# Optimization experiments

Measured on AMD Instinct MI355X. Metric: run time of the kernel, lower is better.

Reference implementation:

```python
import jax, jax.numpy as jnp
import numpy as np

N_SENT = 100000   # source ('sent') nodes
N_TYPE = 10000    # destination ('type') nodes
E = 640000        # edges of etype 'has'
D = 128           # out_dim
LEAKY_SLOPE = 0.01  # F.leaky_relu default


def setup_inputs() -> dict:
    key = jax.random.key(0)
    k0, k1, k2, k3, k4 = jax.random.split(key, 5)
    h_sent = jax.random.normal(k0, (N_SENT, D), jnp.float32)
    h_type = jax.random.normal(k1, (N_TYPE, D), jnp.float32)
    # attn_fc: Linear(2*D, 1, bias=False) -> weight [1, 2*D]
    attn_w = jax.random.normal(k2, (1, 2 * D), jnp.float32) * (1.0 / np.sqrt(2 * D))
    src_idx = jax.random.randint(k3, (E,), 0, N_SENT, dtype=jnp.int32)
    dst_idx = jax.random.randint(k4, (E,), 0, N_TYPE, dtype=jnp.int32)
    return {"h_sent": h_sent, "h_type": h_type, "attn_w": attn_w,
            "src_idx": src_idx, "dst_idx": dst_idx}


def reference(h_sent, h_type, attn_w, src_idx, dst_idx):
    w = attn_w[0]  # [2D]
    # attn_fc(cat(src_h, dst_h)) == src_h @ w[:D] + dst_h @ w[D:]  (no bias)
    s_src = h_sent @ w[:D]   # [N_SENT]
    s_dst = h_type @ w[D:]   # [N_TYPE]
    e = jax.nn.leaky_relu(s_src[src_idx] + s_dst[dst_idx], LEAKY_SLOPE)  # [E]
    # segment (per-destination) softmax over incoming edges
    m = jax.ops.segment_max(e, dst_idx, num_segments=N_TYPE)             # [N_TYPE]
    m = jnp.where(jnp.isfinite(m), m, 0.0)                               # empty segments -> 0
    ex = jnp.exp(e - m[dst_idx])                                         # [E]
    denom = jax.ops.segment_sum(ex, dst_idx, num_segments=N_TYPE)        # [N_TYPE]
    alpha = ex / denom[dst_idx]                                          # [E]
    # weighted scatter-sum of source features into destination nodes
    msg = alpha[:, None] * h_sent[src_idx]                               # [E, D]
    h_new = jax.ops.segment_sum(msg, dst_idx, num_segments=N_TYPE)       # [N_TYPE, D]
    # DGL only updates nodes that received messages; isolated nodes keep h
    deg = jax.ops.segment_sum(jnp.ones_like(e), dst_idx, num_segments=N_TYPE)
    return jnp.where(deg[:, None] > 0, h_new, h_type)
```

## Files before the change

kernel.cpp:

```cpp
#include <hip/hip_runtime.h>
#include <stdint.h>
#include <stddef.h>

#define N_SENT 100000
#define N_TYPE 10000
#define NEDGE  640000
#define NROWS  (N_SENT + N_TYPE)
#define HB     128
#define HCHUNK (NEDGE / HB)

__device__ __forceinline__ float bf2f(uint32_t lo16) {
    return __builtin_bit_cast(float, lo16 << 16);
}
__device__ __forceinline__ uint32_t f2bf(float f) {
    uint32_t u = __builtin_bit_cast(uint32_t, f);
    return (u + 0x7fffu + ((u >> 16) & 1u)) >> 16;
}
__device__ __forceinline__ bool detect_bf16(const uint32_t* __restrict__ h) {
    uint32_t u = h[threadIdx.x & 63];
    uint32_t e_lo = (u >> 7) & 0xffu;
    int ok = (e_lo >= 100u && e_lo <= 140u) ? 1 : 0;
    unsigned long long m = __ballot(ok);
    return __popcll(m) >= 48;
}

#define SCORE_BLOCKS ((NROWS + 63) / 64)

__global__ __launch_bounds__(256) void scores_count_k(const void* __restrict__ h_sent,
                                                      const void* __restrict__ h_type,
                                                      const void* __restrict__ attn_w,
                                                      const int* __restrict__ dst,
                                                      float* __restrict__ s_src,
                                                      float* __restrict__ s_dst,
                                                      uint32_t* __restrict__ count2) {
    __shared__ uint32_t hist[N_TYPE];
    int b = blockIdx.x;
    if (b < SCORE_BLOCKS) {
        int lane = threadIdx.x & 63;
        int r0   = (b * 4 + (int)(threadIdx.x >> 6)) * 16;
        bool isbf = detect_bf16((const uint32_t*)h_sent);
        float v[16];
        if (isbf) {
            uint32_t wv_s = ((const uint32_t*)attn_w)[lane];
            uint32_t wv_t = ((const uint32_t*)attn_w)[64 + lane];
            float ws0 = bf2f(wv_s & 0xffffu), ws1 = bf2f(wv_s >> 16);
            float wt0 = bf2f(wv_t & 0xffffu), wt1 = bf2f(wv_t >> 16);
#pragma unroll
            for (int i = 0; i < 16; i++) {
                int g = r0 + i;
                if (g >= NROWS) { v[i] = 0.0f; continue; }
                bool isSrc = g < N_SENT;
                const uint32_t* hp = isSrc
                    ? (const uint32_t*)h_sent + (size_t)g * 64
                    : (const uint32_t*)h_type + (size_t)(g - N_SENT) * 64;
                uint32_t hv = hp[lane];
                v[i] = isSrc ? (bf2f(hv & 0xffffu) * ws0 + bf2f(hv >> 16) * ws1)
                             : (bf2f(hv & 0xffffu) * wt0 + bf2f(hv >> 16) * wt1);
            }
        } else {
            float2 wv_s = ((const float2*)attn_w)[lane];
            float2 wv_t = ((const float2*)attn_w)[64 + lane];
#pragma unroll
            for (int i = 0; i < 16; i++) {
                int g = r0 + i;
                if (g >= NROWS) { v[i] = 0.0f; continue; }
                bool isSrc = g < N_SENT;
                const float2* hp = isSrc
                    ? (const float2*)h_sent + (size_t)g * 64
                    : (const float2*)h_type + (size_t)(g - N_SENT) * 64;
                float2 hv = hp[lane];
                v[i] = isSrc ? (hv.x * wv_s.x + hv.y * wv_s.y)
                             : (hv.x * wv_t.x + hv.y * wv_t.y);
            }
        }
        int b0 = lane & 1, b1 = (lane >> 1) & 1, b2 = (lane >> 2) & 1, b3 = (lane >> 3) & 1;
        float w_[8];
#pragma unroll
        for (int i = 0; i < 8; i++) {
            float keep = b0 ? v[2 * i + 1] : v[2 * i];
            float send = b0 ? v[2 * i]     : v[2 * i + 1];
            w_[i] = keep + __shfl_xor(send, 1, 64);
        }
        float x_[4];
#pragma unroll
        for (int i = 0; i < 4; i++) {
            float keep = b1 ? w_[2 * i + 1] : w_[2 * i];
            float send = b1 ? w_[2 * i]     : w_[2 * i + 1];
            x_[i] = keep + __shfl_xor(send, 2, 64);
        }
        float y_[2];
#pragma unroll
        for (int i = 0; i < 2; i++) {
            float keep = b2 ? x_[2 * i + 1] : x_[2 * i];
            float send = b2 ? x_[2 * i]     : x_[2 * i + 1];
            y_[i] = keep + __shfl_xor(send, 4, 64);
        }
        float z;
        {
            float keep = b3 ? y_[1] : y_[0];
            float send = b3 ? y_[0] : y_[1];
            z = keep + __shfl_xor(send, 8, 64);
        }
        z += __shfl_xor(z, 16, 64);
        z += __shfl_xor(z, 32, 64);
        if (lane < 16) {
            int g = r0 + lane;
            if (g < NROWS) {
                if (g < N_SENT) s_src[g] = z;
                else            s_dst[g - N_SENT] = z;
            }
        }
    } else {
        int cb = b - SCORE_BLOCKS;
        int t  = threadIdx.x;
        for (int i = t; i < N_TYPE; i += 256) hist[i] = 0u;
        __syncthreads();
        int e0 = cb * HCHUNK;
        for (int i = t; i < HCHUNK; i += 256)
            atomicAdd(&hist[dst[e0 + i]], 1u);
        __syncthreads();
        uint32_t* row = count2 + (size_t)cb * N_TYPE;
        for (int i = t; i < N_TYPE; i += 256) row[i] = hist[i];
    }
}

__global__ __launch_bounds__(256) void sumscan_k(uint32_t* __restrict__ count2,
                                                 uint32_t* __restrict__ total) {
    int b = blockIdx.x * 256 + threadIdx.x;
    if (b >= N_TYPE) return;
    uint32_t run = 0;
#pragma unroll 8
    for (int c = 0; c < HB; c++) {
        uint32_t* p = count2 + (size_t)c * N_TYPE + b;
        uint32_t v = *p;
        *p = run;
        run += v;
    }
    total[b] = run;
}

__global__ __launch_bounds__(1024) void scan_k(const uint32_t* __restrict__ total,
                                               uint32_t* __restrict__ offsets) {
    const int CH = 10;
    int t = threadIdx.x, lane = t & 63, wv = t >> 6;
    int base = t * CH;
    uint32_t local[CH];
    uint32_t tsum = 0;
#pragma unroll
    for (int i = 0; i < CH; i++) {
        int idx = base + i;
        uint32_t c = (idx < N_TYPE) ? total[idx] : 0u;
        local[i] = c;
        tsum += c;
    }
    uint32_t orig = tsum;
#pragma unroll
    for (int off = 1; off < 64; off <<= 1) {
        uint32_t v = __shfl_up(tsum, off, 64);
        if (lane >= off) tsum += v;
    }
    __shared__ uint32_t wsum[16];
    if (lane == 63) wsum[wv] = tsum;
    __syncthreads();
    if (wv == 0 && lane < 16) {
        uint32_t u = wsum[lane], o = u;
#pragma unroll
        for (int off = 1; off < 16; off <<= 1) {
            uint32_t v = __shfl_up(u, off, 64);
            if (lane >= off) u += v;
        }
        wsum[lane] = u - o;
    }
    __syncthreads();
    uint32_t run = wsum[wv] + tsum - orig;
#pragma unroll
    for (int i = 0; i < CH; i++) {
        int idx = base + i;
        if (idx < N_TYPE) {
            offsets[idx] = run;
            run += local[i];
        } else if (idx == N_TYPE) {
            offsets[idx] = run;
        }
    }
}

__global__ __launch_bounds__(256) void fill_k(const int* __restrict__ src,
                                              const int* __restrict__ dst,
                                              const float* __restrict__ s_src,
                                              const float* __restrict__ s_dst,
                                              const uint32_t* __restrict__ offsets,
                                              const uint32_t* __restrict__ base2,
                                              uint2* __restrict__ edata) {
    __shared__ uint32_t cur[N_TYPE];
    int cb = blockIdx.x;
    int t  = threadIdx.x;
    const uint4* off4 = (const uint4*)offsets;
    const uint4* brow4 = (const uint4*)(base2 + (size_t)cb * N_TYPE);
    for (int i = t; i < N_TYPE / 4; i += 256) {
        uint4 o = off4[i], bq = brow4[i];
        cur[4 * i + 0] = o.x + bq.x;
        cur[4 * i + 1] = o.y + bq.y;
        cur[4 * i + 2] = o.z + bq.z;
        cur[4 * i + 3] = o.w + bq.w;
    }
    __syncthreads();
    int e0 = cb * HCHUNK;
    for (int i = t; i < HCHUNK; i += 256) {
        int e = e0 + i;
        int d = dst[e];
        int s = src[e];
        float v = s_src[s] + s_dst[d];
        v = v > 0.0f ? v : 0.01f * v;
        float w = __expf(v);
        uint32_t pos = atomicAdd(&cur[d], 1u);
        edata[pos] = make_uint2((uint32_t)s, __builtin_bit_cast(uint32_t, w));
    }
}

__global__ __launch_bounds__(256) void agg_k(const void* __restrict__ h_sent,
                                             const void* __restrict__ h_type,
                                             const uint32_t* __restrict__ offsets,
                                             const uint2* __restrict__ edata,
                                             void* __restrict__ out) {
    int lane = threadIdx.x & 63;
    int j = (blockIdx.x * 256 + (int)threadIdx.x) >> 6;
    if (j >= N_TYPE) return;
    bool isbf = detect_bf16((const uint32_t*)h_sent);
    uint32_t beg = offsets[j], end = offsets[j + 1];
    if (isbf) {
        int g = lane >> 4, p = lane & 15;
        if (beg == end) {
            if (lane < 16)
                ((uint4*)out)[(size_t)j * 16 + p] = ((const uint4*)h_type)[(size_t)j * 16 + p];
            return;
        }
        const uint4* hp = (const uint4*)h_sent;
        float a[8] = {0, 0, 0, 0, 0, 0, 0, 0};
        float den = 0.0f;
        uint32_t k = beg;
        for (; k + 32 <= end; k += 32) {
            uint2 ed = edata[k + (lane & 31)];
#pragma unroll
            for (int i = 0; i < 8; i++) {
                int sl = 4 * i + g;
                uint32_t s = (uint32_t)__shfl((int)ed.x, sl, 64);
                float    w = __builtin_bit_cast(float, (uint32_t)__shfl((int)ed.y, sl, 64));
                uint4 gv = hp[(size_t)s * 16 + p];
                den += w;
                a[0] += w * bf2f(gv.x & 0xffffu); a[1] += w * bf2f(gv.x >> 16);
                a[2] += w * bf2f(gv.y & 0xffffu); a[3] += w * bf2f(gv.y >> 16);
                a[4] += w * bf2f(gv.z & 0xffffu); a[5] += w * bf2f(gv.z >> 16);
                a[6] += w * bf2f(gv.w & 0xffffu); a[7] += w * bf2f(gv.w >> 16);
            }
        }
        for (; k < end; k += 4) {
            uint32_t idx = k + (uint32_t)g;
            bool valid = idx < end;
            uint2 ed = edata[valid ? idx : (end - 1)];
            float w = valid ? __builtin_bit_cast(float, ed.y) : 0.0f;
            uint4 gv = hp[(size_t)ed.x * 16 + p];
            den += w;
            a[0] += w * bf2f(gv.x & 0xffffu); a[1] += w * bf2f(gv.x >> 16);
            a[2] += w * bf2f(gv.y & 0xffffu); a[3] += w * bf2f(gv.y >> 16);
            a[4] += w * bf2f(gv.z & 0xffffu); a[5] += w * bf2f(gv.z >> 16);
            a[6] += w * bf2f(gv.w & 0xffffu); a[7] += w * bf2f(gv.w >> 16);
        }
#pragma unroll
        for (int i = 0; i < 8; i++) {
            a[i] += __shfl_xor(a[i], 16, 64);
            a[i] += __shfl_xor(a[i], 32, 64);
        }
        den += __shfl_xor(den, 16, 64);
        den += __shfl_xor(den, 32, 64);
        float inv = 1.0f / den;
        if (lane < 16) {
            uint4 o;
            o.x = f2bf(a[0] * inv) | (f2bf(a[1] * inv) << 16);
            o.y = f2bf(a[2] * inv) | (f2bf(a[3] * inv) << 16);
            o.z = f2bf(a[4] * inv) | (f2bf(a[5] * inv) << 16);
            o.w = f2bf(a[6] * inv) | (f2bf(a[7] * inv) << 16);
            ((uint4*)out)[(size_t)j * 16 + p] = o;
        }
    } else {
        int g = lane >> 5, p = lane & 31;
        if (beg == end) {
            if (lane < 32)
                ((float4*)out)[(size_t)j * 32 + p] = ((const float4*)h_type)[(size_t)j * 32 + p];
            return;
        }
        const float4* hp = (const float4*)h_sent;
        float a0 = 0, a1 = 0, a2 = 0, a3 = 0, den = 0.0f;
        uint32_t k = beg;
        for (; k + 16 <= end; k += 16) {
            uint2 ed = edata[k + (lane & 15)];
#pragma unroll
            for (int i = 0; i < 8; i++) {
                int sl = 2 * i + g;
                uint32_t s = (uint32_t)__shfl((int)ed.x, sl, 64);
                float    w = __builtin_bit_cast(float, (uint32_t)__shfl((int)ed.y, sl, 64));
                float4 gv = hp[(size_t)s * 32 + p];
                den += w;
                a0 += w * gv.x; a1 += w * gv.y; a2 += w * gv.z; a3 += w * gv.w;
            }
        }
        for (; k < end; k += 2) {
            uint32_t idx = k + (uint32_t)g;
            bool valid = idx < end;
            uint2 ed = edata[valid ? idx : (end - 1)];
            float w = valid ? __builtin_bit_cast(float, ed.y) : 0.0f;
            float4 gv = hp[(size_t)ed.x * 32 + p];
            den += w;
            a0 += w * gv.x; a1 += w * gv.y; a2 += w * gv.z; a3 += w * gv.w;
        }
        a0 += __shfl_xor(a0, 32, 64);
        a1 += __shfl_xor(a1, 32, 64);
        a2 += __shfl_xor(a2, 32, 64);
        a3 += __shfl_xor(a3, 32, 64);
        den += __shfl_xor(den, 32, 64);
        float inv = 1.0f / den;
        if (lane < 32)
            ((float4*)out)[(size_t)j * 32 + p] = make_float4(a0 * inv, a1 * inv, a2 * inv, a3 * inv);
    }
}

static inline size_t align_up(size_t x) { return (x + 255) & ~(size_t)255; }

extern "C" void kernel_launch(void* const* d_in, const int* in_sizes, int n_in,
                              void* d_out, int out_size, void* d_ws, size_t ws_size,
                              hipStream_t stream) {
    const void* h_sent = d_in[0];
    const void* h_type = d_in[1];
    const void* attn_w = d_in[2];
    const int* src_idx = (const int*)d_in[3];
    const int* dst_idx = (const int*)d_in[4];

    char* w = (char*)d_ws;
    float*    s_src   = (float*)w;    w += align_up((size_t)N_SENT * 4);
    float*    s_dst   = (float*)w;    w += align_up((size_t)N_TYPE * 4);
    uint32_t* count2  = (uint32_t*)w; w += align_up((size_t)HB * N_TYPE * 4);
    uint32_t* total   = (uint32_t*)w; w += align_up((size_t)N_TYPE * 4);
    uint32_t* offsets = (uint32_t*)w; w += align_up((size_t)(N_TYPE + 1) * 4);
    uint2*    edata   = (uint2*)w;    w += align_up((size_t)NEDGE * 8);

    scores_count_k<<<SCORE_BLOCKS + HB, 256, 0, stream>>>(
        h_sent, h_type, attn_w, dst_idx, s_src, s_dst, count2);
    sumscan_k<<<(N_TYPE + 255) / 256, 256, 0, stream>>>(count2, total);
    scan_k<<<1, 1024, 0, stream>>>(total, offsets);
    fill_k<<<HB, 256, 0, stream>>>(src_idx, dst_idx, s_src, s_dst, offsets, count2, edata);
    agg_k<<<(N_TYPE + 3) / 4, 256, 0, stream>>>(h_sent, h_type, offsets, edata, d_out);
}
```

Before: 203.7 us.

## Fuse all five stages into one cooperative persistent kernel with grid syncs

Replaces the five separate launches (scores+histogram, column scan, total scan, fill, aggregate) with a single cooperative kernel of 512 persistent blocks that separates the phases with grid.sync, and loops over score rows and aggregation nodes with grid-stride loops. The goal is to remove per-launch overhead and the idle gaps between small kernels. It also packs the per-block histogram into 16-bit halves, halving LDS use for the atomics. In exchange, grid-wide barriers cost time, the fixed grid may under-occupy the aggregation phase, and the single-block scan adds a serial step.

```diff
diff --git a/kernel.cpp b/kernel.cpp
--- a/kernel.cpp
+++ b/kernel.cpp
@@ -1,13 +1,19 @@
 #include <hip/hip_runtime.h>
+#include <hip/hip_cooperative_groups.h>
 #include <stdint.h>
 #include <stddef.h>
+
+namespace cg = cooperative_groups;
 
 #define N_SENT 100000
 #define N_TYPE 10000
 #define NEDGE  640000
 #define NROWS  (N_SENT + N_TYPE)
+#define NB     512
+#define SCOREB 384
 #define HB     128
 #define HCHUNK (NEDGE / HB)
+#define NTASK  ((NROWS + 15) / 16)
 
 __device__ __forceinline__ float bf2f(uint32_t lo16) {
     return __builtin_bit_cast(float, lo16 << 16);
@@ -24,303 +30,324 @@
     return __popcll(m) >= 48;
 }
 
-#define SCORE_BLOCKS ((NROWS + 63) / 64)
-
-__global__ __launch_bounds__(256) void scores_count_k(const void* __restrict__ h_sent,
-                                                      const void* __restrict__ h_type,
-                                                      const void* __restrict__ attn_w,
-                                                      const int* __restrict__ dst,
-                                                      float* __restrict__ s_src,
-                                                      float* __restrict__ s_dst,
-                                                      uint32_t* __restrict__ count2) {
-    __shared__ uint32_t hist[N_TYPE];
-    int b = blockIdx.x;
-    if (b < SCORE_BLOCKS) {
-        int lane = threadIdx.x & 63;
-        int r0   = (b * 4 + (int)(threadIdx.x >> 6)) * 16;
-        bool isbf = detect_bf16((const uint32_t*)h_sent);
-        float v[16];
+__global__ __launch_bounds__(256, 4) void mega_k(
+    const void* __restrict__ h_sent, const void* __restrict__ h_type,
+    const void* __restrict__ attn_w,
+    const int* __restrict__ src_idx, const int* __restrict__ dst_idx,
+    float* __restrict__ s_src, float* __restrict__ s_dst,
+    uint32_t* __restrict__ count2, uint32_t* __restrict__ offsets,
+    uint2* __restrict__ edata, void* __restrict__ out)
+{
+    __shared__ uint32_t lds[N_TYPE];
+    cg::grid_group grid = cg::this_grid();
+    const int t    = threadIdx.x;
+    const int lane = t & 63;
+    const int wvid = t >> 6;
+    const int b    = blockIdx.x;
+    const bool isbf = detect_bf16((const uint32_t*)h_sent);
+
+    if (b < SCOREB) {
         if (isbf) {
             uint32_t wv_s = ((const uint32_t*)attn_w)[lane];
             uint32_t wv_t = ((const uint32_t*)attn_w)[64 + lane];
             float ws0 = bf2f(wv_s & 0xffffu), ws1 = bf2f(wv_s >> 16);
             float wt0 = bf2f(wv_t & 0xffffu), wt1 = bf2f(wv_t >> 16);
-#pragma unroll
-            for (int i = 0; i < 16; i++) {
-                int g = r0 + i;
-                if (g >= NROWS) { v[i] = 0.0f; continue; }
-                bool isSrc = g < N_SENT;
-                const uint32_t* hp = isSrc
-                    ? (const uint32_t*)h_sent + (size_t)g * 64
-                    : (const uint32_t*)h_type + (size_t)(g - N_SENT) * 64;
-                uint32_t hv = hp[lane];
-                v[i] = isSrc ? (bf2f(hv & 0xffffu) * ws0 + bf2f(hv >> 16) * ws1)
-                             : (bf2f(hv & 0xffffu) * wt0 + bf2f(hv >> 16) * wt1);
+            for (int task = b * 4 + wvid; task < NTASK; task += SCOREB * 4) {
+                int r0 = task * 16;
+                float v[16];
+#pragma unroll
+                for (int i = 0; i < 16; i++) {
+                    int g = r0 + i;
+                    if (g >= NROWS) { v[i] = 0.0f; continue; }
+                    bool isSrc = g < N_SENT;
+                    const uint32_t* hp = isSrc
+                        ? (const uint32_t*)h_sent + (size_t)g * 64
+                        : (const uint32_t*)h_type + (size_t)(g - N_SENT) * 64;
+                    uint32_t hv = hp[lane];
+                    v[i] = isSrc ? (bf2f(hv & 0xffffu) * ws0 + bf2f(hv >> 16) * ws1)
+                                 : (bf2f(hv & 0xffffu) * wt0 + bf2f(hv >> 16) * wt1);
+                }
+                int b0 = lane & 1, b1 = (lane >> 1) & 1, b2 = (lane >> 2) & 1, b3 = (lane >> 3) & 1;
+                float w_[8];
+#pragma unroll
+                for (int i = 0; i < 8; i++) {
+                    float keep = b0 ? v[2 * i + 1] : v[2 * i];
+                    float send = b0 ? v[2 * i]     : v[2 * i + 1];
+                    w_[i] = keep + __shfl_xor(send, 1, 64);
+                }
+                float x_[4];
+#pragma unroll
+                for (int i = 0; i < 4; i++) {
+                    float keep = b1 ? w_[2 * i + 1] : w_[2 * i];
+                    float send = b1 ? w_[2 * i]     : w_[2 * i + 1];
+                    x_[i] = keep + __shfl_xor(send, 2, 64);
+                }
+                float y_[2];
+#pragma unroll
+                for (int i = 0; i < 2; i++) {
+                    float keep = b2 ? x_[2 * i + 1] : x_[2 * i];
+                    float send = b2 ? x_[2 * i]     : x_[2 * i + 1];
+                    y_[i] = keep + __shfl_xor(send, 4, 64);
+                }
+                float z;
+                {
+                    float keep = b3 ? y_[1] : y_[0];
+                    float send = b3 ? y_[0] : y_[1];
+                    z = keep + __shfl_xor(send, 8, 64);
+                }
+                z += __shfl_xor(z, 16, 64);
+                z += __shfl_xor(z, 32, 64);
+                if (lane < 16) {
+                    int g = r0 + lane;
+                    if (g < NROWS) {
+                        if (g < N_SENT) s_src[g] = z;
+                        else            s_dst[g - N_SENT] = z;
+                    }
+                }
             }
         } else {
             float2 wv_s = ((const float2*)attn_w)[lane];
             float2 wv_t = ((const float2*)attn_w)[64 + lane];
-#pragma unroll
-            for (int i = 0; i < 16; i++) {
-                int g = r0 + i;
-                if (g >= NROWS) { v[i] = 0.0f; continue; }
-                bool isSrc = g < N_SENT;
-                const float2* hp = isSrc
-                    ? (const float2*)h_sent + (size_t)g * 64
-                    : (const float2*)h_type + (size_t)(g - N_SENT) * 64;
-                float2 hv = hp[lane];
-                v[i] = isSrc ? (hv.x * wv_s.x + hv.y * wv_s.y)
-                             : (hv.x * wv_t.x + hv.y * wv_t.y);
-            }
-        }
-        int b0 = lane & 1, b1 = (lane >> 1) & 1, b2 = (lane >> 2) & 1, b3 = (lane >> 3) & 1;
-        float w_[8];
-#pragma unroll
-        for (int i = 0; i < 8; i++) {
-            float keep = b0 ? v[2 * i + 1] : v[2 * i];
-            float send = b0 ? v[2 * i]     : v[2 * i + 1];
-            w_[i] = keep + __shfl_xor(send, 1, 64);
-        }
-        float x_[4];
-#pragma unroll
-        for (int i = 0; i < 4; i++) {
-            float keep = b1 ? w_[2 * i + 1] : w_[2 * i];
-            float send = b1 ? w_[2 * i]     : w_[2 * i + 1];
-            x_[i] = keep + __shfl_xor(send, 2, 64);
-        }
-        float y_[2];
-#pragma unroll
-        for (int i = 0; i < 2; i++) {
-            float keep = b2 ? x_[2 * i + 1] : x_[2 * i];
-            float send = b2 ? x_[2 * i]     : x_[2 * i + 1];
-            y_[i] = keep + __shfl_xor(send, 4, 64);
-        }
-        float z;
-        {
-            float keep = b3 ? y_[1] : y_[0];
-            float send = b3 ? y_[0] : y_[1];
-            z = keep + __shfl_xor(send, 8, 64);
-        }
-        z += __shfl_xor(z, 16, 64);
-        z += __shfl_xor(z, 32, 64);
-        if (lane < 16) {
-            int g = r0 + lane;
-            if (g < NROWS) {
-                if (g < N_SENT) s_src[g] = z;
-                else            s_dst[g - N_SENT] = z;
+            for (int task = b * 4 + wvid; task < NTASK; task += SCOREB * 4) {
+                int r0 = task * 16;
+                float v[16];
+#pragma unroll
+                for (int i = 0; i < 16; i++) {
+                    int g = r0 + i;
+                    if (g >= NROWS) { v[i] = 0.0f; continue; }
+                    bool isSrc = g < N_SENT;
+                    const float2* hp = isSrc
+                        ? (const float2*)h_sent + (size_t)g * 64
+                        : (const float2*)h_type + (size_t)(g - N_SENT) * 64;
+                    float2 hv = hp[lane];
+                    v[i] = isSrc ? (hv.x * wv_s.x + hv.y * wv_s.y)
+                                 : (hv.x * wv_t.x + hv.y * wv_t.y);
+                }
+                int b0 = lane & 1, b1 = (lane >> 1) & 1, b2 = (lane >> 2) & 1, b3 = (lane >> 3) & 1;
+                float w_[8];
+#pragma unroll
+                for (int i = 0; i < 8; i++) {
+                    float keep = b0 ? v[2 * i + 1] : v[2 * i];
+                    float send = b0 ? v[2 * i]     : v[2 * i + 1];
+                    w_[i] = keep + __shfl_xor(send, 1, 64);
+                }
+                float x_[4];
+#pragma unroll
+                for (int i = 0; i < 4; i++) {
+                    float keep = b1 ? w_[2 * i + 1] : w_[2 * i];
+                    float send = b1 ? w_[2 * i]     : w_[2 * i + 1];
+                    x_[i] = keep + __shfl_xor(send, 2, 64);
+                }
+                float y_[2];
+#pragma unroll
+                for (int i = 0; i < 2; i++) {
+                    float keep = b2 ? x_[2 * i + 1] : x_[2 * i];
+                    float send = b2 ? x_[2 * i]     : x_[2 * i + 1];
+                    y_[i] = keep + __shfl_xor(send, 4, 64);
+                }
+                float z;
+                {
+                    float keep = b3 ? y_[1] : y_[0];
+                    float send = b3 ? y_[0] : y_[1];
+                    z = keep + __shfl_xor(send, 8, 64);
+                }
+                z += __shfl_xor(z, 16, 64);
+                z += __shfl_xor(z, 32, 64);
+                if (lane < 16) {
+                    int g = r0 + lane;
+                    if (g < NROWS) {
+                        if (g < N_SENT) s_src[g] = z;
+                        else            s_dst[g - N_SENT] = z;
+                    }
+                }
             }
         }
     } else {
-        int cb = b - SCORE_BLOCKS;
-        int t  = threadIdx.x;
-        for (int i = t; i < N_TYPE; i += 256) hist[i] = 0u;
+        int cb = b - SCOREB;
+        for (int i = t; i < N_TYPE / 2; i += 256) lds[i] = 0u;
         __syncthreads();
         int e0 = cb * HCHUNK;
-        for (int i = t; i < HCHUNK; i += 256)
-            atomicAdd(&hist[dst[e0 + i]], 1u);
+        for (int i = t; i < HCHUNK; i += 256) {
+            int d = dst_idx[e0 + i];
+            atomicAdd(&lds[d >> 1], 1u << ((d & 1) * 16));
+        }
         __syncthreads();
-        uint32_t* row = count2 + (size_t)cb * N_TYPE;
-        for (int i = t; i < N_TYPE; i += 256) row[i] = hist[i];
-    }
-}
-
-__global__ __launch_bounds__(256) void sumscan_k(uint32_t* __restrict__ count2,
-                                                 uint32_t* __restrict__ total) {
-    int b = blockIdx.x * 256 + threadIdx.x;
-    if (b >= N_TYPE) return;
-    uint32_t run = 0;
-#pragma unroll 8
-    for (int c = 0; c < HB; c++) {
-        uint32_t* p = count2 + (size_t)c * N_TYPE + b;
-        uint32_t v = *p;
-        *p = run;
-        run += v;
-    }
-    total[b] = run;
-}
-
-__global__ __launch_bounds__(1024) void scan_k(const uint32_t* __restrict__ total,
-                                               uint32_t* __restrict__ offsets) {
-    const int CH = 10;
-    int t = threadIdx.x, lane = t & 63, wv = t >> 6;
-    int base = t * CH;
-    uint32_t local[CH];
-    uint32_t tsum = 0;
-#pragma unroll
-    for (int i = 0; i < CH; i++) {
-        int idx = base + i;
-        uint32_t c = (idx < N_TYPE) ? total[idx] : 0u;
-        local[i] = c;
-        tsum += c;
-    }
-    uint32_t orig = tsum;
-#pragma unroll
-    for (int off = 1; off < 64; off <<= 1) {
-        uint32_t v = __shfl_up(tsum, off, 64);
-        if (lane >= off) tsum += v;
-    }
-    __shared__ uint32_t wsum[16];
-    if (lane == 63) wsum[wv] = tsum;
-    __syncthreads();
-    if (wv == 0 && lane < 16) {
-        uint32_t u = wsum[lane], o = u;
-#pragma unroll
-        for (int off = 1; off < 16; off <<= 1) {
-            uint32_t v = __shfl_up(u, off, 64);
-            if (lane >= off) u += v;
-        }
-        wsum[lane] = u - o;
-    }
-    __syncthreads();
-    uint32_t run = wsum[wv] + tsum - orig;
-#pragma unroll
-    for (int i = 0; i < CH; i++) {
-        int idx = base + i;
-        if (idx < N_TYPE) {
-            offsets[idx] = run;
-            run += local[i];
-        } else if (idx == N_TYPE) {
-            offsets[idx] = run;
-        }
-    }
-}
-
-__global__ __launch_bounds__(256) void fill_k(const int* __restrict__ src,
-                                              const int* __restrict__ dst,
-                                              const float* __restrict__ s_src,
-                                              const float* __restrict__ s_dst,
-                                              const uint32_t* __restrict__ offsets,
-                                              const uint32_t* __restrict__ base2,
-                                              uint2* __restrict__ edata) {
-    __shared__ uint32_t cur[N_TYPE];
-    int cb = blockIdx.x;
-    int t  = threadIdx.x;
-    const uint4* off4 = (const uint4*)offsets;
-    const uint4* brow4 = (const uint4*)(base2 + (size_t)cb * N_TYPE);
-    for (int i = t; i < N_TYPE / 4; i += 256) {
-        uint4 o = off4[i], bq = brow4[i];
-        cur[4 * i + 0] = o.x + bq.x;
-        cur[4 * i + 1] = o.y + bq.y;
-        cur[4 * i + 2] = o.z + bq.z;
-        cur[4 * i + 3] = o.w + bq.w;
-    }
-    __syncthreads();
-    int e0 = cb * HCHUNK;
-    for (int i = t; i < HCHUNK; i += 256) {
-        int e = e0 + i;
-        int d = dst[e];
-        int s = src[e];
-        float v = s_src[s] + s_dst[d];
-        v = v > 0.0f ? v : 0.01f * v;
-        float w = __expf(v);
-        uint32_t pos = atomicAdd(&cur[d], 1u);
-        edata[pos] = make_uint2((uint32_t)s, __builtin_bit_cast(uint32_t, w));
-    }
-}
-
-__global__ __launch_bounds__(256) void agg_k(const void* __restrict__ h_sent,
-                                             const void* __restrict__ h_type,
-                                             const uint32_t* __restrict__ offsets,
-                                             const uint2* __restrict__ edata,
-                                             void* __restrict__ out) {
-    int lane = threadIdx.x & 63;
-    int j = (blockIdx.x * 256 + (int)threadIdx.x) >> 6;
-    if (j >= N_TYPE) return;
-    bool isbf = detect_bf16((const uint32_t*)h_sent);
-    uint32_t beg = offsets[j], end = offsets[j + 1];
-    if (isbf) {
-        int g = lane >> 4, p = lane & 15;
-        if (beg == end) {
-            if (lane < 16)
-                ((uint4*)out)[(size_t)j * 16 + p] = ((const uint4*)h_type)[(size_t)j * 16 + p];
-            return;
-        }
-        const uint4* hp = (const uint4*)h_sent;
-        float a[8] = {0, 0, 0, 0, 0, 0, 0, 0};
-        float den = 0.0f;
-        uint32_t k = beg;
-        for (; k + 32 <= end; k += 32) {
-            uint2 ed = edata[k + (lane & 31)];
-#pragma unroll
-            for (int i = 0; i < 8; i++) {
-                int sl = 4 * i + g;
-                uint32_t s = (uint32_t)__shfl((int)ed.x, sl, 64);
-                float    w = __builtin_bit_cast(float, (uint32_t)__shfl((int)ed.y, sl, 64));
-                uint4 gv = hp[(size_t)s * 16 + p];
+        uint2* row2 = (uint2*)(count2 + (size_t)cb * N_TYPE);
+        for (int i = t; i < N_TYPE / 2; i += 256) {
+            uint32_t wd = lds[i];
+            row2[i] = make_uint2(wd & 0xffffu, wd >> 16);
+        }
+    }
+    grid.sync();
+
+    {
+        int gtid = b * 256 + t;
+        if (gtid < N_TYPE) {
+            uint32_t run = 0;
+            for (int c = 0; c < HB; c++) {
+                uint32_t* p = count2 + (size_t)c * N_TYPE + gtid;
+                uint32_t v = *p;
+                *p = run;
+                run += v;
+            }
+            offsets[gtid] = run;
+        }
+    }
+    grid.sync();
+
+    if (b == 0) {
+        const int CH = N_TYPE / 256 + 1;
+        int base = t * CH;
+        uint32_t tsum = 0;
+        for (int i = 0; i < CH; i++) {
+            int idx = base + i;
+            if (idx < N_TYPE) tsum += offsets[idx];
+        }
+        uint32_t inc = tsum;
+#pragma unroll
+        for (int off = 1; off < 64; off <<= 1) {
+            uint32_t u = __shfl_up(inc, off, 64);
+            if (lane >= off) inc += u;
+        }
+        if (lane == 63) lds[wvid] = inc;
+        __syncthreads();
+        uint32_t wpre = 0;
+        for (int i = 0; i < wvid; i++) wpre += lds[i];
+        uint32_t run = wpre + inc - tsum;
+        for (int i = 0; i < CH; i++) {
+            int idx = base + i;
+            if (idx < N_TYPE) {
+                uint32_t v = offsets[idx];
+                offsets[idx] = run;
+                run += v;
+            } else if (idx == N_TYPE) {
+                offsets[idx] = run;
+            }
+        }
+    }
+    grid.sync();
+
+    if (b < HB) {
+        const uint4* off4 = (const uint4*)offsets;
+        const uint4* b4   = (const uint4*)(count2 + (size_t)b * N_TYPE);
+        for (int i = t; i < N_TYPE / 4; i += 256) {
+            uint4 o = off4[i], q = b4[i];
+            lds[4 * i + 0] = o.x + q.x;
+            lds[4 * i + 1] = o.y + q.y;
+            lds[4 * i + 2] = o.z + q.z;
+            lds[4 * i + 3] = o.w + q.w;
+        }
+        __syncthreads();
+        int e0 = b * HCHUNK;
+        for (int i = t; i < HCHUNK; i += 256) {
+            int e = e0 + i;
+            int d = dst_idx[e];
+            int s = src_idx[e];
+            float v = s_src[s] + s_dst[d];
+            v = v > 0.0f ? v : 0.01f * v;
+            float w = __expf(v);
+            uint32_t pos = atomicAdd(&lds[d], 1u);
+            edata[pos] = make_uint2((uint32_t)s, __builtin_bit_cast(uint32_t, w));
+        }
+    }
+    grid.sync();
+
+    for (int j = b * 4 + wvid; j < N_TYPE; j += NB * 4) {
+        uint32_t beg = offsets[j], end = offsets[j + 1];
+        if (isbf) {
+            int g = lane >> 4, p = lane & 15;
+            if (beg == end) {
+                if (lane < 16)
+                    ((uint4*)out)[(size_t)j * 16 + p] = ((const uint4*)h_type)[(size_t)j * 16 + p];
+                continue;
+            }
+            const uint4* hp = (const uint4*)h_sent;
+            float a[8] = {0, 0, 0, 0, 0, 0, 0, 0};
+            float den = 0.0f;
+            uint32_t k = beg;
+            for (; k + 32 <= end; k += 32) {
+                uint2 ed = edata[k + (lane & 31)];
+#pragma unroll
+                for (int i = 0; i < 8; i++) {
+                    int sl = 4 * i + g;
+                    uint32_t s = (uint32_t)__shfl((int)ed.x, sl, 64);
+                    float    w = __builtin_bit_cast(float, (uint32_t)__shfl((int)ed.y, sl, 64));
+                    uint4 gv = hp[(size_t)s * 16 + p];
+                    den += w;
+                    a[0] += w * bf2f(gv.x & 0xffffu); a[1] += w * bf2f(gv.x >> 16);
+                    a[2] += w * bf2f(gv.y & 0xffffu); a[3] += w * bf2f(gv.y >> 16);
+                    a[4] += w * bf2f(gv.z & 0xffffu); a[5] += w * bf2f(gv.z >> 16);
+                    a[6] += w * bf2f(gv.w & 0xffffu); a[7] += w * bf2f(gv.w >> 16);
+                }
+            }
+            for (; k < end; k += 4) {
+                uint32_t idx = k + (uint32_t)g;
+                bool valid = idx < end;
+                uint2 ed = edata[valid ? idx : (end - 1)];
+                float w = valid ? __builtin_bit_cast(float, ed.y) : 0.0f;
+                uint4 gv = hp[(size_t)ed.x * 16 + p];
                 den += w;
                 a[0] += w * bf2f(gv.x & 0xffffu); a[1] += w * bf2f(gv.x >> 16);
                 a[2] += w * bf2f(gv.y & 0xffffu); a[3] += w * bf2f(gv.y >> 16);
                 a[4] += w * bf2f(gv.z & 0xffffu); a[5] += w * bf2f(gv.z >> 16);
                 a[6] += w * bf2f(gv.w & 0xffffu); a[7] += w * bf2f(gv.w >> 16);
             }
-        }
-        for (; k < end; k += 4) {
-            uint32_t idx = k + (uint32_t)g;
-            bool valid = idx < end;
-            uint2 ed = edata[valid ? idx : (end - 1)];
-            float w = valid ? __builtin_bit_cast(float, ed.y) : 0.0f;
-            uint4 gv = hp[(size_t)ed.x * 16 + p];
-            den += w;
-            a[0] += w * bf2f(gv.x & 0xffffu); a[1] += w * bf2f(gv.x >> 16);
-            a[2] += w * bf2f(gv.y & 0xffffu); a[3] += w * bf2f(gv.y >> 16);
-            a[4] += w * bf2f(gv.z & 0xffffu); a[5] += w * bf2f(gv.z >> 16);
-            a[6] += w * bf2f(gv.w & 0xffffu); a[7] += w * bf2f(gv.w >> 16);
-        }
-#pragma unroll
-        for (int i = 0; i < 8; i++) {
-            a[i] += __shfl_xor(a[i], 16, 64);
-            a[i] += __shfl_xor(a[i], 32, 64);
-        }
-        den += __shfl_xor(den, 16, 64);
-        den += __shfl_xor(den, 32, 64);
-        float inv = 1.0f / den;
-        if (lane < 16) {
-            uint4 o;
-            o.x = f2bf(a[0] * inv) | (f2bf(a[1] * inv) << 16);
-            o.y = f2bf(a[2] * inv) | (f2bf(a[3] * inv) << 16);
-            o.z = f2bf(a[4] * inv) | (f2bf(a[5] * inv) << 16);
-            o.w = f2bf(a[6] * inv) | (f2bf(a[7] * inv) << 16);
-            ((uint4*)out)[(size_t)j * 16 + p] = o;
-        }
-    } else {
-        int g = lane >> 5, p = lane & 31;
-        if (beg == end) {
-            if (lane < 32)
-                ((float4*)out)[(size_t)j * 32 + p] = ((const float4*)h_type)[(size_t)j * 32 + p];
-            return;
-        }
-        const float4* hp = (const float4*)h_sent;
-        float a0 = 0, a1 = 0, a2 = 0, a3 = 0, den = 0.0f;
-        uint32_t k = beg;
-        for (; k + 16 <= end; k += 16) {
-            uint2 ed = edata[k + (lane & 15)];
 #pragma unroll
             for (int i = 0; i < 8; i++) {
-                int sl = 2 * i + g;
-                uint32_t s = (uint32_t)__shfl((int)ed.x, sl, 64);
-                float    w = __builtin_bit_cast(float, (uint32_t)__shfl((int)ed.y, sl, 64));
-                float4 gv = hp[(size_t)s * 32 + p];
+                a[i] += __shfl_xor(a[i], 16, 64);
+                a[i] += __shfl_xor(a[i], 32, 64);
+            }
+            den += __shfl_xor(den, 16, 64);
+            den += __shfl_xor(den, 32, 64);
+            float inv = 1.0f / den;
+            if (lane < 16) {
+                uint4 o;
+                o.x = f2bf(a[0] * inv) | (f2bf(a[1] * inv) << 16);
+                o.y = f2bf(a[2] * inv) | (f2bf(a[3] * inv) << 16);
+                o.z = f2bf(a[4] * inv) | (f2bf(a[5] * inv) << 16);
+                o.w = f2bf(a[6] * inv) | (f2bf(a[7] * inv) << 16);
+                ((uint4*)out)[(size_t)j * 16 + p] = o;
+            }
+        } else {
+            int g = lane >> 5, p = lane & 31;
+            if (beg == end) {
+                if (lane < 32)
+                    ((float4*)out)[(size_t)j * 32 + p] = ((const float4*)h_type)[(size_t)j * 32 + p];
+                continue;
+            }
+            const float4* hp = (const float4*)h_sent;
+            float a0 = 0, a1 = 0, a2 = 0, a3 = 0, den = 0.0f;
+            uint32_t k = beg;
+            for (; k + 16 <= end; k += 16) {
+                uint2 ed = edata[k + (lane & 15)];
+#pragma unroll
+                for (int i = 0; i < 8; i++) {
+                    int sl = 2 * i + g;
+                    uint32_t s = (uint32_t)__shfl((int)ed.x, sl, 64);
+                    float    w = __builtin_bit_cast(float, (uint32_t)__shfl((int)ed.y, sl, 64));
+                    float4 gv = hp[(size_t)s * 32 + p];
+                    den += w;
+                    a0 += w * gv.x; a1 += w * gv.y; a2 += w * gv.z; a3 += w * gv.w;
+                }
+            }
+            for (; k < end; k += 2) {
+                uint32_t idx = k + (uint32_t)g;
+                bool valid = idx < end;
+                uint2 ed = edata[valid ? idx : (end - 1)];
+                float w = valid ? __builtin_bit_cast(float, ed.y) : 0.0f;
+                float4 gv = hp[(size_t)ed.x * 32 + p];
                 den += w;
                 a0 += w * gv.x; a1 += w * gv.y; a2 += w * gv.z; a3 += w * gv.w;
             }
-        }
-        for (; k < end; k += 2) {
-            uint32_t idx = k + (uint32_t)g;
-            bool valid = idx < end;
-            uint2 ed = edata[valid ? idx : (end - 1)];
-            float w = valid ? __builtin_bit_cast(float, ed.y) : 0.0f;
-            float4 gv = hp[(size_t)ed.x * 32 + p];
-            den += w;
-            a0 += w * gv.x; a1 += w * gv.y; a2 += w * gv.z; a3 += w * gv.w;
-        }
-        a0 += __shfl_xor(a0, 32, 64);
-        a1 += __shfl_xor(a1, 32, 64);
-        a2 += __shfl_xor(a2, 32, 64);
-        a3 += __shfl_xor(a3, 32, 64);
-        den += __shfl_xor(den, 32, 64);
-        float inv = 1.0f / den;
-        if (lane < 32)
-            ((float4*)out)[(size_t)j * 32 + p] = make_float4(a0 * inv, a1 * inv, a2 * inv, a3 * inv);
+            a0 += __shfl_xor(a0, 32, 64);
+            a1 += __shfl_xor(a1, 32, 64);
+            a2 += __shfl_xor(a2, 32, 64);
+            a3 += __shfl_xor(a3, 32, 64);
+            den += __shfl_xor(den, 32, 64);
+            float inv = 1.0f / den;
+            if (lane < 32)
+                ((float4*)out)[(size_t)j * 32 + p] = make_float4(a0 * inv, a1 * inv, a2 * inv, a3 * inv);
+        }
     }
 }
 
@@ -334,19 +361,20 @@
     const void* attn_w = d_in[2];
     const int* src_idx = (const int*)d_in[3];
     const int* dst_idx = (const int*)d_in[4];
+    void* outp = d_out;
 
     char* w = (char*)d_ws;
     float*    s_src   = (float*)w;    w += align_up((size_t)N_SENT * 4);
     float*    s_dst   = (float*)w;    w += align_up((size_t)N_TYPE * 4);
     uint32_t* count2  = (uint32_t*)w; w += align_up((size_t)HB * N_TYPE * 4);
-    uint32_t* total   = (uint32_t*)w; w += align_up((size_t)N_TYPE * 4);
     uint32_t* offsets = (uint32_t*)w; w += align_up((size_t)(N_TYPE + 1) * 4);
     uint2*    edata   = (uint2*)w;    w += align_up((size_t)NEDGE * 8);
 
-    scores_count_k<<<SCORE_BLOCKS + HB, 256, 0, stream>>>(
-        h_sent, h_type, attn_w, dst_idx, s_src, s_dst, count2);
-    sumscan_k<<<(N_TYPE + 255) / 256, 256, 0, stream>>>(count2, total);
-    scan_k<<<1, 1024, 0, stream>>>(total, offsets);
-    fill_k<<<HB, 256, 0, stream>>>(src_idx, dst_idx, s_src, s_dst, offsets, count2, edata);
-    agg_k<<<(N_TYPE + 3) / 4, 256, 0, stream>>>(h_sent, h_type, offsets, edata, d_out);
-}
+    void* args[] = { (void*)&h_sent, (void*)&h_type, (void*)&attn_w,
+                     (void*)&src_idx, (void*)&dst_idx,
+                     (void*)&s_src, (void*)&s_dst,
+                     (void*)&count2, (void*)&offsets,
+                     (void*)&edata, (void*)&outp };
+    hipLaunchCooperativeKernel((const void*)mega_k, dim3(NB), dim3(256),
+                               args, 0, stream);
+}
```

Result: slower. 442.4 us (+117.1%).
